# Kernel tuning notes

Hardware: AMD Instinct MI355X
Metric: run time of the kernel (lower is better)

Reference implementation:

```python
import jax, jax.numpy as jnp
import numpy as np

N_USER = 20000
N_ITEM = 20000
N = N_USER + N_ITEM          # total nodes
D = 128                      # n_hid (= in_feats = out_feats)
H = 4                        # GAT heads
L = 2                        # n_layers
M = 8                        # mem_size (hypernet bottleneck)
T = 5                        # num_rels in MemoryLayer
E_UI = 40000                 # user->item bipartite edges
E_T = 16000                  # homogeneous edges per relation type (grouped)
EPS = 1e-5


def _layer_norm(x, w, b):
    mu = x.mean(-1, keepdims=True)
    var = ((x - mu) ** 2).mean(-1, keepdims=True)
    return (x - mu) * jax.lax.rsqrt(var + EPS) * w + b


def _gat(h_src, h_dst, src_idx, dst_idx, n_dst, W, al, ar, bias):
    """DGL GATConv (shared fc, eval-mode dropout=identity, elu activation)."""
    fs = (h_src @ W.T).reshape(-1, H, D)          # [Ns, H, D]
    fd = (h_dst @ W.T).reshape(-1, H, D)          # [Nd, H, D]
    el = (fs * al).sum(-1)                        # [Ns, H]
    er = (fd * ar).sum(-1)                        # [Nd, H]
    e = jax.nn.leaky_relu(el[src_idx] + er[dst_idx], 0.2)   # [E, H]
    emax = jax.ops.segment_max(e, dst_idx, num_segments=n_dst)
    ex = jnp.exp(e - emax[dst_idx])
    denom = jax.ops.segment_sum(ex, dst_idx, num_segments=n_dst)
    a = ex / denom[dst_idx]                       # edge softmax per dst
    rst = jax.ops.segment_sum(a[:, :, None] * fs[src_idx], dst_idx, num_segments=n_dst)
    return jax.nn.elu(rst + bias.reshape(1, H, D))           # [Nd, H, D]


def _memory_layer(feat, edge_src, edge_dst, Wc, bc, Ww, nWc, nbc, nWw, h_bias, ln_w, ln_b):
    # edges grouped by relation type: edge_src/edge_dst are [T, E_T]
    hs = feat[edge_src]                           # [T, Et, D]
    hd = feat[edge_dst]                           # [T, Et, D]
    # per-edge hypernetwork: coef = LeakyReLU(Linear(dst)); w = Ww(coef); msg = w @ src
    coef = jax.nn.leaky_relu(jnp.einsum('ted,tmd->tem', hd, Wc) + bc[:, None, :], 0.2)
    tmp = jnp.einsum('tei,tmoi->temo', hs, Ww)    # [T, Et, M, D] -- M-bottleneck path
    msg = jnp.einsum('tem,temo->teo', coef, tmp)  # [T, Et, D]
    flat_dst = edge_dst.reshape(-1)
    s = jax.ops.segment_sum(msg.reshape(-1, D), flat_dst, num_segments=N)
    cnt = jax.ops.segment_sum(jnp.ones((flat_dst.shape[0],), feat.dtype), flat_dst, num_segments=N)
    agg = s / jnp.maximum(cnt, 1.0)[:, None]      # fn.mean (0 for isolated nodes)
    rep = _layer_norm(agg, ln_w, ln_b) + h_bias
    # self-loop node_ME(feat, feat)
    ncoef = jax.nn.leaky_relu(feat @ nWc.T + nbc, 0.2)       # [N, M]
    ntmp = jnp.einsum('ni,moi->nmo', feat, nWw)              # [N, M, D]
    rep = rep + jnp.einsum('nm,nmo->no', ncoef, ntmp)
    return jax.nn.leaky_relu(rep, 0.2)            # dropout = identity (eval)


def setup_inputs() -> dict:
    key = jax.random.key(0)
    ks = jax.random.split(key, 16)
    s = 0.05
    return {
        "embedding": jax.random.normal(ks[0], (N, D), jnp.float32),
        "gat_fc_W": jax.random.normal(ks[1], (L, 2, H * D, D), jnp.float32) * s,
        "gat_attn_l": jax.random.normal(ks[2], (L, 2, H, D), jnp.float32) * s,
        "gat_attn_r": jax.random.normal(ks[3], (L, 2, H, D), jnp.float32) * s,
        "gat_bias": jnp.zeros((L, 2, H * D), jnp.float32),
        "proj_W": jax.random.normal(ks[4], (L, 2, D, H * D), jnp.float32) * s,
        "proj_b": jnp.zeros((L, 2, D), jnp.float32),
        "mem_rel_Wc": jax.random.normal(ks[5], (L, T, M, D), jnp.float32) * s,
        "mem_rel_bc": jnp.zeros((L, T, M), jnp.float32),
        "mem_rel_Ww": jax.random.normal(ks[6], (L, T, M, D, D), jnp.float32) * s,
        "mem_node_Wc": jax.random.normal(ks[7], (L, M, D), jnp.float32) * s,
        "mem_node_bc": jnp.zeros((L, M), jnp.float32),
        "mem_node_Ww": jax.random.normal(ks[8], (L, M, D, D), jnp.float32) * s,
        "mem_h_bias": jnp.zeros((L, D), jnp.float32),
        "mem_ln_w": jnp.ones((L, D), jnp.float32),
        "mem_ln_b": jnp.zeros((L, D), jnp.float32),
        "final_ln_w": jnp.ones(((L + 1) * D,), jnp.float32),
        "final_ln_b": jnp.zeros(((L + 1) * D,), jnp.float32),
        "src_u": jax.random.randint(ks[9], (E_UI,), 0, N_USER, jnp.int32),
        "dst_i": jax.random.randint(ks[10], (E_UI,), 0, N_ITEM, jnp.int32),
        "edge_src": jax.random.randint(ks[11], (T, E_T), 0, N, jnp.int32),
        "edge_dst": jax.random.randint(ks[12], (T, E_T), 0, N, jnp.int32),
    }


def reference(embedding, gat_fc_W, gat_attn_l, gat_attn_r, gat_bias, proj_W, proj_b,
              mem_rel_Wc, mem_rel_bc, mem_rel_Ww, mem_node_Wc, mem_node_bc, mem_node_Ww,
              mem_h_bias, mem_ln_w, mem_ln_b, final_ln_w, final_ln_b,
              src_u, dst_i, edge_src, edge_dst):
    features = embedding
    all_emb = [features]
    for l in range(L):
        hu, hi = features[:N_USER], features[N_USER:]
        # relation 0: item -> user (dst = user)
        gu = _gat(hi, hu, dst_i, src_u, N_USER,
                  gat_fc_W[l, 0], gat_attn_l[l, 0], gat_attn_r[l, 0], gat_bias[l, 0])
        ru = jax.nn.elu(gu.reshape(N_USER, H * D) @ proj_W[l, 0].T + proj_b[l, 0])
        # relation 1: user -> item (dst = item)
        gi = _gat(hu, hi, src_u, dst_i, N_ITEM,
                  gat_fc_W[l, 1], gat_attn_l[l, 1], gat_attn_r[l, 1], gat_bias[l, 1])
        ri = jnp.asarray(jax.nn.elu(gi.reshape(N_ITEM, H * D) @ proj_W[l, 1].T + proj_b[l, 1]))
        trans = jnp.concatenate([ru, ri], axis=0)             # [N, D]
        mem = _memory_layer(all_emb[-1], edge_src, edge_dst,
                            mem_rel_Wc[l], mem_rel_bc[l], mem_rel_Ww[l],
                            mem_node_Wc[l], mem_node_bc[l], mem_node_Ww[l],
                            mem_h_bias[l], mem_ln_w[l], mem_ln_b[l])
        features = mem + trans
        all_emb.append(features)
    return _layer_norm(jnp.concatenate(all_emb, axis=1), final_ln_w, final_ln_b)
```

## Files before the change

kernel.cpp:

```cpp
#include <hip/hip_runtime.h>
#include <hip/hip_bf16.h>
#include <math.h>

typedef __hip_bfloat16 bf16;

#define NUSER 20000
#define NITEM 20000
#define NTOT  40000
#define DD    128
#define HH    4
#define TT    5
#define MMEM  8
#define EUI   40000
#define ET    16000

#define MP_N  40064
#define MP_H  20096

typedef __attribute__((ext_vector_type(8))) short short8;
typedef __attribute__((ext_vector_type(4))) float f32x4;

__device__ __forceinline__ void gload16(const bf16* g, bf16* l){
  __builtin_amdgcn_global_load_lds(
      (const __attribute__((address_space(1))) unsigned int*)g,
      (__attribute__((address_space(3))) unsigned int*)l, 16, 0, 0);
}
__device__ __forceinline__ float bu2f_lo(unsigned u){ return __uint_as_float(u << 16); }
__device__ __forceinline__ float bu2f_hi(unsigned u){ return __uint_as_float(u & 0xffff0000u); }

__device__ __forceinline__ int stage_cg(int lane){
  return (((lane&3) ^ ((lane>>2)&3) ^ (lane>>4)) << 3);
}
__device__ __forceinline__ int read_pc8(int lm, int lq){
  return ((lq ^ (lm&3) ^ ((lm>>2)&3)) << 3);
}

__global__ __launch_bounds__(256) void k_mfma_gemm(
    const bf16* __restrict__ A, const bf16* __restrict__ B,
    const float* __restrict__ bias, float* __restrict__ C,
    long Astr, long Bstr, long biasStr, long Cstr,
    int ldc, int M, int K, int act, int accum)
{
  A += (size_t)blockIdx.z*Astr; B += (size_t)blockIdx.z*Bstr;
  if (bias) bias += (size_t)blockIdx.z*biasStr;
  C += (size_t)blockIdx.z*Cstr;
  __shared__ bf16 As[128*32];
  __shared__ bf16 Bs[128*32];
  int tid = threadIdx.x;
  int wave = tid >> 6, lane = tid & 63;
  int r0 = blockIdx.x * 128, c0 = blockIdx.y * 128;
  int wm = (wave >> 1) * 64, wn = (wave & 1) * 64;
  f32x4 acc[4][4];
  #pragma unroll
  for (int i=0;i<4;i++)
    #pragma unroll
    for (int j=0;j<4;j++) acc[i][j] = (f32x4){0.f,0.f,0.f,0.f};

  int rq = lane >> 2;
  int cg = stage_cg(lane);
  const bf16* Ag = A + (size_t)(r0 + wave*32 + rq)*K + cg;
  const bf16* Bg = B + (size_t)(c0 + wave*32 + rq)*K + cg;
  bf16* AsW = As + wave*32*32;
  bf16* BsW = Bs + wave*32*32;
  int lm = lane & 15, lq = lane >> 4;
  int pc8 = read_pc8(lm, lq);
  const bf16* Ard = As + (wm + lm)*32 + pc8;
  const bf16* Brd = Bs + (wn + lm)*32 + pc8;

  for (int k0 = 0; k0 < K; k0 += 32){
    gload16(Ag + k0,            AsW);
    gload16(Ag + 16*K + k0,     AsW + 16*32);
    gload16(Bg + k0,            BsW);
    gload16(Bg + 16*K + k0,     BsW + 16*32);
    __syncthreads();
    short8 af[4], bfv[4];
    #pragma unroll
    for (int i=0;i<4;i++) af[i]  = *(const short8*)(Ard + i*16*32);
    #pragma unroll
    for (int j=0;j<4;j++) bfv[j] = *(const short8*)(Brd + j*16*32);
    #pragma unroll
    for (int i=0;i<4;i++)
      #pragma unroll
      for (int j=0;j<4;j++)
        acc[i][j] = __builtin_amdgcn_mfma_f32_16x16x32_bf16(af[i], bfv[j], acc[i][j], 0, 0, 0);
    __syncthreads();
  }
  #pragma unroll
  for (int i=0;i<4;i++){
    #pragma unroll
    for (int j=0;j<4;j++){
      int c = c0 + wn + j*16 + lm;
      #pragma unroll
      for (int rg=0; rg<4; rg++){
        int r = r0 + wm + i*16 + lq*4 + rg;
        if (r < M){
          float v = acc[i][j][rg];
          if (bias) v += bias[c];
          if (act==1) v = v>0.f ? v : expm1f(v);
          float* cp = &C[(size_t)r*ldc + c];
          if (accum) *cp += v; else *cp = v;
        }
      }
    }
  }
}

__global__ __launch_bounds__(256) void k_fc_gemm(
    const bf16* __restrict__ A, const bf16* __restrict__ B,
    bf16* __restrict__ Fb, const float* __restrict__ al, const float* __restrict__ ar,
    float* __restrict__ el, float* __restrict__ er, int M)
{
  __shared__ bf16 As[128*32];
  __shared__ bf16 Bs[128*32];
  __shared__ float redE[2][2][128];
  int tid = threadIdx.x;
  int wave = tid >> 6, lane = tid & 63;
  int h = blockIdx.y;
  int r0 = blockIdx.x * 128;
  int wm = (wave >> 1) * 64, wn = (wave & 1) * 64;
  f32x4 acc[4][4];
  #pragma unroll
  for (int i=0;i<4;i++)
    #pragma unroll
    for (int j=0;j<4;j++) acc[i][j] = (f32x4){0.f,0.f,0.f,0.f};

  int rq = lane >> 2;
  int cg = stage_cg(lane);
  const bf16* Ag = A + (size_t)(r0 + wave*32 + rq)*128 + cg;
  const bf16* Bg = B + (size_t)(h*128 + wave*32 + rq)*128 + cg;
  bf16* AsW = As + wave*32*32;
  bf16* BsW = Bs + wave*32*32;
  int lm = lane & 15, lq = lane >> 4;
  int pc8 = read_pc8(lm, lq);
  const bf16* Ard = As + (wm + lm)*32 + pc8;
  const bf16* Brd = Bs + (wn + lm)*32 + pc8;

  for (int k0 = 0; k0 < 128; k0 += 32){
    gload16(Ag + k0,             AsW);
    gload16(Ag + 16*128 + k0,    AsW + 16*32);
    gload16(Bg + k0,             BsW);
    gload16(Bg + 16*128 + k0,    BsW + 16*32);
    __syncthreads();
    short8 af[4], bfv[4];
    #pragma unroll
    for (int i=0;i<4;i++) af[i]  = *(const short8*)(Ard + i*16*32);
    #pragma unroll
    for (int j=0;j<4;j++) bfv[j] = *(const short8*)(Brd + j*16*32);
    #pragma unroll
    for (int i=0;i<4;i++)
      #pragma unroll
      for (int j=0;j<4;j++)
        acc[i][j] = __builtin_amdgcn_mfma_f32_16x16x32_bf16(af[i], bfv[j], acc[i][j], 0, 0, 0);
    __syncthreads();
  }
  float alv[4], arv[4];
  #pragma unroll
  for (int j=0;j<4;j++){
    int c = h*128 + wn + j*16 + lm;
    alv[j] = al[c]; arv[j] = ar[c];
  }
  int wnh = wave & 1;
  #pragma unroll
  for (int i=0;i<4;i++){
    #pragma unroll
    for (int rg=0; rg<4; rg++){
      float se = 0.f, sr = 0.f;
      #pragma unroll
      for (int j=0;j<4;j++){
        float v = acc[i][j][rg];
        se = fmaf(v, alv[j], se);
        sr = fmaf(v, arv[j], sr);
      }
      #pragma unroll
      for (int msk=1; msk<16; msk<<=1){
        se += __shfl_xor(se, msk);
        sr += __shfl_xor(sr, msk);
      }
      if (lm == 0){
        int rl = wm + i*16 + lq*4 + rg;
        redE[0][wnh][rl] = se;
        redE[1][wnh][rl] = sr;
      }
    }
  }
  #pragma unroll
  for (int i=0;i<4;i++){
    #pragma unroll
    for (int j=0;j<4;j++){
      int c = h*128 + wn + j*16 + lm;
      #pragma unroll
      for (int rg=0; rg<4; rg++){
        int r = r0 + wm + i*16 + lq*4 + rg;
        if (r < M) Fb[(size_t)r*512 + c] = __float2bfloat16(acc[i][j][rg]);
      }
    }
  }
  __syncthreads();
  if (tid < 128){
    int r = r0 + tid;
    if (r < M) el[(size_t)r*4 + h] = redE[0][0][tid] + redE[0][1][tid];
  } else {
    int t2 = tid - 128;
    int r = r0 + t2;
    if (r < M) er[(size_t)r*4 + h] = redE[1][0][t2] + redE[1][1][t2];
  }
}

__global__ __launch_bounds__(256) void k_memgemm(
    const float* __restrict__ feat, const int* __restrict__ src,
    const float* __restrict__ coef, const bf16* __restrict__ B,
    float* __restrict__ C, bf16* __restrict__ Cb,
    const float* __restrict__ trans, float* __restrict__ fout,
    long srcStr, long coefStr, long Bstr, long CbStr,
    int Mvalid, int mode)
{
  __shared__ bf16 Af[64*144];
  __shared__ float cfS[8*64];
  __shared__ bf16 Bs[2][128*32];
  int t = blockIdx.y;
  const int*   srcT  = src ? src + (size_t)t*srcStr : nullptr;
  const float* coefT = coef + (size_t)t*coefStr;
  const bf16*  Bt    = B + (size_t)t*Bstr;
  int tid = threadIdx.x, wave = tid >> 6, lane = tid & 63;
  int r0 = blockIdx.x * 64;

  {
    int rL = tid >> 2, seg = tid & 3;
    int r = r0 + rL;
    bool valid = r < Mvalid;
    int s = valid ? (srcT ? srcT[r] : r) : 0;
    const float4* fp = (const float4*)(feat + (size_t)s*128 + seg*32);
    bf16* ap = Af + rL*144 + seg*32;
    #pragma unroll
    for (int q=0;q<8;q+=2){
      float4 v0 = fp[q], v1 = fp[q+1];
      __hip_bfloat162 p0 = __float22bfloat162_rn(make_float2(v0.x, v0.y));
      __hip_bfloat162 p1 = __float22bfloat162_rn(make_float2(v0.z, v0.w));
      __hip_bfloat162 p2 = __float22bfloat162_rn(make_float2(v1.x, v1.y));
      __hip_bfloat162 p3 = __float22bfloat162_rn(make_float2(v1.z, v1.w));
      *(__hip_bfloat162*)(ap + q*4)     = p0;
      *(__hip_bfloat162*)(ap + q*4 + 2) = p1;
      *(__hip_bfloat162*)(ap + q*4 + 4) = p2;
      *(__hip_bfloat162*)(ap + q*4 + 6) = p3;
    }
  }
  if (tid < 64){
    int r = r0 + tid;
    bool valid = r < Mvalid;
    #pragma unroll
    for (int m=0;m<8;m++)
      cfS[m*64 + tid] = valid ? coefT[(size_t)r*8 + m] : 0.f;
  }

  int rq = lane >> 2;
  int cg = stage_cg(lane);
  const bf16* Bg0 = Bt + (size_t)(wave*32 + rq)*1024 + cg;
  const bf16* Bg1 = Bt + (size_t)(wave*32 + 16 + rq)*1024 + cg;

  int wm = (wave >> 1) * 32, wn = (wave & 1) * 64;
  int lm = lane & 15, lq = lane >> 4;
  int pc8 = read_pc8(lm, lq);

  f32x4 accC[2][4];
  #pragma unroll
  for (int i=0;i<2;i++)
    #pragma unroll
    for (int j=0;j<4;j++) accC[i][j] = (f32x4){0.f,0.f,0.f,0.f};

  {
    bf16* d = Bs[0] + wave*1024;
    gload16(Bg0, d);
    gload16(Bg1, d + 512);
  }
  __syncthreads();

  int buf = 0;
  #pragma unroll
  for (int m = 0; m < 8; m++){
    f32x4 accM[2][4];
    #pragma unroll
    for (int ic = 0; ic < 4; ic++){
      int kk = m*4 + ic;
      if (kk + 1 < 32){
        int k1 = (kk + 1) * 32;
        bf16* d = Bs[buf^1] + wave*1024;
        gload16(Bg0 + k1, d);
        gload16(Bg1 + k1, d + 512);
      }
      short8 af[2], bfv[4];
      #pragma unroll
      for (int i=0;i<2;i++)
        af[i] = *(const short8*)(Af + (size_t)(wm + i*16 + lm)*144 + ic*32 + lq*8);
      #pragma unroll
      for (int j=0;j<4;j++)
        bfv[j] = *(const short8*)(Bs[buf] + (wn + lm + j*16)*32 + pc8);
      if (ic == 0){
        #pragma unroll
        for (int i=0;i<2;i++)
          #pragma unroll
          for (int j=0;j<4;j++)
            accM[i][j] = __builtin_amdgcn_mfma_f32_16x16x32_bf16(af[i], bfv[j],
                             (f32x4){0.f,0.f,0.f,0.f}, 0, 0, 0);
      } else {
        #pragma unroll
        for (int i=0;i<2;i++)
          #pragma unroll
          for (int j=0;j<4;j++)
            accM[i][j] = __builtin_amdgcn_mfma_f32_16x16x32_bf16(af[i], bfv[j], accM[i][j], 0, 0, 0);
      }
      __syncthreads();
      buf ^= 1;
    }
    #pragma unroll
    for (int i=0;i<2;i++){
      f32x4 cf4 = *(const f32x4*)(cfS + m*64 + wm + i*16 + lq*4);
      #pragma unroll
      for (int j=0;j<4;j++)
        #pragma unroll
        for (int rg=0; rg<4; rg++)
          accC[i][j][rg] = fmaf(cf4[rg], accM[i][j][rg], accC[i][j][rg]);
    }
  }
  #pragma unroll
  for (int i=0;i<2;i++){
    #pragma unroll
    for (int j=0;j<4;j++){
      int c = wn + j*16 + lm;
      #pragma unroll
      for (int rg=0; rg<4; rg++){
        int r = r0 + wm + i*16 + lq*4 + rg;
        if (r < Mvalid){
          float v = accC[i][j][rg];
          if (mode == 0){
            Cb[(size_t)t*CbStr + (size_t)r*128 + c] = __float2bfloat16(v);
          } else {
            float x = C[(size_t)r*128 + c] + v;
            x = x>0.f ? x : 0.2f*x;
            fout[(size_t)r*128 + c] = x + trans[(size_t)r*128 + c];
          }
        }
      }
    }
  }
}

__global__ void k_f2b(const float* __restrict__ in, bf16* __restrict__ o, int nv, int nt){
  int i = blockIdx.x*256 + threadIdx.x;
  if (i < nt) o[i] = __float2bfloat16(i < nv ? in[i] : 0.f);
}

__global__ void k_repack(const float* __restrict__ in, bf16* __restrict__ o){
  int s = blockIdx.y;
  int g = blockIdx.x*256 + threadIdx.x;
  int m = g >> 14, od = (g >> 7) & 127, i = g & 127;
  o[(size_t)s*131072 + (size_t)od*1024 + m*128 + i] = __float2bfloat16(in[(size_t)s*131072 + g]);
}

__global__ void k_hist(const int* __restrict__ dIdx, int* __restrict__ cnt, int E){
  int e = blockIdx.x*256+threadIdx.x;
  if (e<E) atomicAdd(&cnt[dIdx[e]], 1);
}

__global__ __launch_bounds__(1024) void k_scan(const int* __restrict__ in,
                                               int* __restrict__ out, int n){
  __shared__ int wsum[16];
  __shared__ int carry;
  int tidx = threadIdx.x, lane = tidx & 63, w = tidx >> 6;
  if (tidx == 0) carry = 0;
  __syncthreads();
  for (int base = 0; base < n; base += 1024){
    int i = base + tidx;
    int v = (i < n) ? in[i] : 0;
    int x = v;
    #pragma unroll
    for (int off = 1; off < 64; off <<= 1){
      int t = __shfl_up(x, off);
      if (lane >= off) x += t;
    }
    if (lane == 63) wsum[w] = x;
    __syncthreads();
    if (w == 0 && lane < 16){
      int t = wsum[lane];
      #pragma unroll
      for (int off=1; off<16; off<<=1){
        int u = __shfl_up(t, off, 16);
        if (lane >= off) t += u;
      }
      wsum[lane] = t;
    }
    __syncthreads();
    int woff = (w == 0) ? 0 : wsum[w-1];
    int excl = carry + woff + x - v;
    if (i < n) out[i] = excl;
    __syncthreads();
    if (tidx == 1023) carry = carry + wsum[15];
    __syncthreads();
  }
  if (tidx == 0) out[n] = carry;
}

__global__ void k_csr_scatter(const int* __restrict__ sIdx, const int* __restrict__ dIdx,
                              int sOff, const int* __restrict__ rowptr,
                              int* __restrict__ cursor, int* __restrict__ col, int E){
  int e = blockIdx.x*256+threadIdx.x; if (e>=E) return;
  int d = dIdx[e];
  int pos = rowptr[d] + atomicAdd(&cursor[d], 1);
  col[pos] = sIdx[e] + sOff;
}

__global__ void k_csr_scatter_eid(const int* __restrict__ dIdx, const int* __restrict__ rowptr,
                                  int* __restrict__ cursor, int* __restrict__ col, int E){
  int e = blockIdx.x*256+threadIdx.x; if (e>=E) return;
  int d = dIdx[e];
  int pos = rowptr[d] + atomicAdd(&cursor[d], 1);
  col[pos] = e;
}

__global__ __launch_bounds__(64) void k_gat_gather(
    const int* __restrict__ rowptr, const int* __restrict__ col,
    const float* __restrict__ el, const float* __restrict__ er,
    const bf16* __restrict__ Fb, const float* __restrict__ gb,
    bf16* __restrict__ rstb, int dOff)
{
  int dl = blockIdx.x;
  int lane = threadIdx.x;
  int h = lane >> 4;
  int off = (lane & 15) << 3;
  float erh = er[(size_t)(dl + dOff)*4 + h];
  float m = -INFINITY, den = 0.f;
  float acc[8];
  #pragma unroll
  for (int i=0;i<8;i++) acc[i]=0.f;
  int jb = rowptr[dl], je = rowptr[dl+1];
  for (int j=jb; j<je; j++){
    int s = col[j];
    float e = el[(size_t)s*4+h] + erh;
    e = e > 0.f ? e : 0.2f*e;
    float mn = fmaxf(m, e);
    float sc = __expf(m - mn);
    float wj = __expf(e - mn);
    den = den*sc + wj;
    m = mn;
    uint4 u = *(const uint4*)(Fb + (size_t)s*512 + h*128 + off);
    acc[0]=acc[0]*sc + wj*bu2f_lo(u.x); acc[1]=acc[1]*sc + wj*bu2f_hi(u.x);
    acc[2]=acc[2]*sc + wj*bu2f_lo(u.y); acc[3]=acc[3]*sc + wj*bu2f_hi(u.y);
    acc[4]=acc[4]*sc + wj*bu2f_lo(u.z); acc[5]=acc[5]*sc + wj*bu2f_hi(u.z);
    acc[6]=acc[6]*sc + wj*bu2f_lo(u.w); acc[7]=acc[7]*sc + wj*bu2f_hi(u.w);
  }
  float inv = den > 0.f ? 1.f/den : 0.f;
  int cb = h*128 + off;
  float x[8];
  #pragma unroll
  for (int q=0;q<8;q++){
    float v = acc[q]*inv + gb[cb+q];
    x[q] = v>0.f ? v : expm1f(v);
  }
  union { uint4 u; __hip_bfloat162 p[4]; } O;
  #pragma unroll
  for (int q=0;q<4;q++) O.p[q] = __float22bfloat162_rn(make_float2(x[2*q], x[2*q+1]));
  *(uint4*)(rstb + (size_t)dl*512 + cb) = O.u;
}

__global__ void k_coef(const float* __restrict__ feat, const int* __restrict__ idx,
                       const float* __restrict__ Wc, const float* __restrict__ bc,
                       float* __restrict__ outc, int cnt){
  int t = blockIdx.y;
  __shared__ float wS[MMEM*DD];
  __shared__ float bS[MMEM];
  for (int i=threadIdx.x;i<MMEM*DD;i+=128) wS[i] = Wc[(size_t)t*MMEM*DD + i];
  if (threadIdx.x < MMEM) bS[threadIdx.x] = bc[t*MMEM + threadIdx.x];
  __syncthreads();
  int e = blockIdx.x*128 + threadIdx.x; if (e >= cnt) return;
  int node = idx ? idx[(size_t)t*cnt + e] : e;
  float acc[MMEM];
  #pragma unroll
  for (int m=0;m<MMEM;m++) acc[m]=bS[m];
  const float* fr = feat + (size_t)node*DD;
  for (int d2=0; d2<DD; d2++){
    float v = fr[d2];
    #pragma unroll
    for (int m=0;m<MMEM;m++) acc[m] = fmaf(v, wS[m*DD+d2], acc[m]);
  }
  float* op = outc + ((size_t)t*cnt + e)*MMEM;
  #pragma unroll
  for (int m=0;m<MMEM;m++){ float v=acc[m]; op[m] = v>0.f ? v : 0.2f*v; }
}

__global__ void k_mem_gather(const int* __restrict__ rpT, const int* __restrict__ colT,
                             const bf16* __restrict__ msg, float* __restrict__ sAgg){
  int n = blockIdx.x*4 + (threadIdx.x >> 6);
  if (n >= NTOT) return;
  int lane = threadIdx.x & 63;
  int jb = rpT[n], je = rpT[n+1];
  float a0=0.f, a1=0.f;
  for (int j=jb;j<je;j++){
    unsigned u = ((const unsigned*)(msg + (size_t)colT[j]*128))[lane];
    a0 += bu2f_lo(u); a1 += bu2f_hi(u);
  }
  *(float2*)(sAgg + (size_t)n*128 + lane*2) = make_float2(a0, a1);
}

__global__ void k_memln(const float* __restrict__ s, const int* __restrict__ rpT,
                        const float* __restrict__ lw, const float* __restrict__ lb,
                        const float* __restrict__ hb, float* __restrict__ outp){
  int n = blockIdx.x, lane = threadIdx.x;
  float c = fmaxf((float)(rpT[n+1]-rpT[n]), 1.f);
  float x1 = s[(size_t)n*128+lane]/c, x2 = s[(size_t)n*128+64+lane]/c;
  float t = x1+x2;
  #pragma unroll
  for (int off=32;off;off>>=1) t += __shfl_xor(t,off);
  float mu = t * (1.f/128.f);
  float d1=x1-mu, d2=x2-mu;
  float v = d1*d1+d2*d2;
  #pragma unroll
  for (int off=32;off;off>>=1) v += __shfl_xor(v,off);
  float r = rsqrtf(v*(1.f/128.f) + 1e-5f);
  outp[(size_t)n*128+lane]    = d1*r*lw[lane]    + lb[lane]    + hb[lane];
  outp[(size_t)n*128+64+lane] = d2*r*lw[64+lane] + lb[64+lane] + hb[64+lane];
}

__global__ void k_final_ln(const float* __restrict__ emb, const float* __restrict__ f1,
                           const float* __restrict__ f2, const float* __restrict__ w,
                           const float* __restrict__ b, float* __restrict__ out){
  int n = blockIdx.x, t = threadIdx.x;
  __shared__ float red[4];
  float x0 = emb[(size_t)n*128+t];
  float x1 = f1[(size_t)n*128+t];
  float x2 = f2[(size_t)n*128+t];
  float s = x0+x1+x2;
  #pragma unroll
  for (int off=32;off;off>>=1) s += __shfl_xor(s,off);
  if ((t&63)==0) red[t>>6] = s;
  __syncthreads();
  float mu = (red[0]+red[1]) * (1.f/384.f);
  float d0=x0-mu, d1=x1-mu, d2=x2-mu;
  float v = d0*d0+d1*d1+d2*d2;
  #pragma unroll
  for (int off=32;off;off>>=1) v += __shfl_xor(v,off);
  if ((t&63)==0) red[2+(t>>6)] = v;
  __syncthreads();
  float var = (red[2]+red[3]) * (1.f/384.f);
  float r = rsqrtf(var + 1e-5f);
  size_t o = (size_t)n*384;
  out[o+t]     = d0*r*w[t]     + b[t];
  out[o+128+t] = d1*r*w[128+t] + b[128+t];
  out[o+256+t] = d2*r*w[256+t] + b[256+t];
}

extern "C" void kernel_launch(void* const* d_in, const int* in_sizes, int n_in,
                              void* d_out, int out_size, void* d_ws, size_t ws_size,
                              hipStream_t stream)
{
  const float* emb   = (const float*)d_in[0];
  const float* fcW   = (const float*)d_in[1];
  const float* attl  = (const float*)d_in[2];
  const float* attr  = (const float*)d_in[3];
  const float* gbias = (const float*)d_in[4];
  const float* projW = (const float*)d_in[5];
  const float* projB = (const float*)d_in[6];
  const float* relWc = (const float*)d_in[7];
  const float* relbc = (const float*)d_in[8];
  const float* relWw = (const float*)d_in[9];
  const float* nodWc = (const float*)d_in[10];
  const float* nodbc = (const float*)d_in[11];
  const float* nodWw = (const float*)d_in[12];
  const float* hbias = (const float*)d_in[13];
  const float* mlnw  = (const float*)d_in[14];
  const float* mlnb  = (const float*)d_in[15];
  const float* flnw  = (const float*)d_in[16];
  const float* flnb  = (const float*)d_in[17];
  const int*  srcU  = (const int*)d_in[18];
  const int*  dstI  = (const int*)d_in[19];
  const int*  eSrc  = (const int*)d_in[20];
  const int*  eDst  = (const int*)d_in[21];
  float* out = (float*)d_out;

  char* wp = (char*)d_ws;
  auto alloc = [&](size_t bytes)->void* {
    void* p = (void*)wp; wp += (bytes + 511) & ~(size_t)511; return p;
  };
  float* feat1 = (float*)alloc((size_t)NTOT*DD*4);
  float* feat2 = (float*)alloc((size_t)NTOT*DD*4);
  float* Fbuf  = (float*)alloc((size_t)NTOT*512*4);
  float* rst   = (float*)alloc((size_t)NTOT*DD*2*4);
  bf16*  rstb0 = (bf16*)alloc((size_t)2*MP_H*512*2);
  float* trans = (float*)alloc((size_t)NTOT*DD*4);
  float* elF   = (float*)alloc((size_t)NTOT*4*4);
  float* erF   = (float*)alloc((size_t)NTOT*4*4);
  int* rpA  = (int*)alloc((size_t)(NUSER+1)*4);
  int* colA = (int*)alloc((size_t)EUI*4);
  int* rpB  = (int*)alloc((size_t)(NITEM+1)*4);
  int* colB = (int*)alloc((size_t)EUI*4);
  int* icnt = (int*)alloc((size_t)20000*4);
  int* icur = (int*)alloc((size_t)20000*4);
  int* rpT  = (int*)alloc((size_t)(NTOT+1)*4);
  int* colT = (int*)alloc((size_t)TT*ET*4);
  int* cntT = (int*)alloc((size_t)NTOT*4);
  int* icurT= (int*)alloc((size_t)NTOT*4);
  bf16* featb  = (bf16*)alloc((size_t)MP_N*DD*2);
  bf16* fcWb   = (bf16*)alloc((size_t)4*512*DD*2);
  bf16* projWb = (bf16*)alloc((size_t)4*DD*512*2);
  bf16* relWwb = (bf16*)alloc((size_t)10*DD*1024*2);
  bf16* nodWwb = (bf16*)alloc((size_t)2*DD*1024*2);
  bf16*  Fb     = (bf16*)Fbuf;
  bf16*  msgBb  = (bf16*)((char*)Fbuf + (size_t)NTOT*512*2);
  float* coefB  = (float*)((char*)msgBb + (size_t)TT*ET*128*2);
  float* ncoefB = coefB + (size_t)TT*ET*8;
  bf16*  rstb1  = rstb0 + (size_t)MP_H*512;
  float* sAgg   = rst;
  float* memO   = rst + (size_t)NTOT*DD;

  k_f2b<<<dim3((4*512*DD+255)/256),256,0,stream>>>(fcW, fcWb, 4*512*DD, 4*512*DD);
  k_f2b<<<dim3((4*DD*512+255)/256),256,0,stream>>>(projW, projWb, 4*DD*512, 4*DD*512);
  k_repack<<<dim3(512,10),256,0,stream>>>(relWw, relWwb);
  k_repack<<<dim3(512,2),256,0,stream>>>(nodWw, nodWwb);
  hipMemsetAsync(rstb0 + (size_t)20000*512, 0, (size_t)(MP_H-20000)*512*2, stream);
  hipMemsetAsync(rstb1 + (size_t)20000*512, 0, (size_t)(MP_H-20000)*512*2, stream);

  hipMemsetAsync(icnt, 0, 20000*4, stream);
  hipMemsetAsync(icur, 0, 20000*4, stream);
  k_hist<<<dim3((EUI+255)/256),256,0,stream>>>(srcU, icnt, EUI);
  k_scan<<<dim3(1),1024,0,stream>>>(icnt, rpA, NUSER);
  k_csr_scatter<<<dim3((EUI+255)/256),256,0,stream>>>(dstI, srcU, NUSER, rpA, icur, colA, EUI);
  hipMemsetAsync(icnt, 0, 20000*4, stream);
  hipMemsetAsync(icur, 0, 20000*4, stream);
  k_hist<<<dim3((EUI+255)/256),256,0,stream>>>(dstI, icnt, EUI);
  k_scan<<<dim3(1),1024,0,stream>>>(icnt, rpB, NITEM);
  k_csr_scatter<<<dim3((EUI+255)/256),256,0,stream>>>(srcU, dstI, 0, rpB, icur, colB, EUI);
  hipMemsetAsync(cntT, 0, NTOT*4, stream);
  hipMemsetAsync(icurT, 0, NTOT*4, stream);
  k_hist<<<dim3((TT*ET+255)/256),256,0,stream>>>(eDst, cntT, TT*ET);
  k_scan<<<dim3(1),1024,0,stream>>>(cntT, rpT, NTOT);
  k_csr_scatter_eid<<<dim3((TT*ET+255)/256),256,0,stream>>>(eDst, rpT, icurT, colT, TT*ET);

  const float* feats[3] = {emb, feat1, feat2};
  for (int l=0; l<2; l++){
    const float* fin  = feats[l];
    float* fout = (float*)feats[l+1];

    k_f2b<<<dim3((MP_N*DD+255)/256),256,0,stream>>>(fin, featb, NTOT*DD, MP_N*DD);

    for (int d=0; d<2; d++){
      k_fc_gemm<<<dim3(MP_N/128, 4),256,0,stream>>>(
          featb, fcWb + (size_t)(l*2+d)*512*DD, Fb,
          attl+(size_t)(l*2+d)*512, attr+(size_t)(l*2+d)*512, elF, erF, NTOT);
      int dOff = (d==0) ? 0 : NUSER;
      const int* rp  = (d==0) ? rpA : rpB;
      const int* col = (d==0) ? colA : colB;
      k_gat_gather<<<dim3(20000),64,0,stream>>>(rp, col, elF, erF, Fb,
          gbias+(size_t)(l*2+d)*512, (d==0) ? rstb0 : rstb1, dOff);
    }
    k_mfma_gemm<<<dim3(MP_H/128, 1, 2),256,0,stream>>>(
        rstb0, projWb + (size_t)(l*2)*DD*512, projB + (size_t)(l*2)*DD, trans,
        (long)MP_H*512, (long)DD*512, (long)DD, (long)20000*DD,
        DD, 20000, 512, 1, 0);

    k_coef<<<dim3((ET+127)/128, TT),128,0,stream>>>(fin, eDst,
        relWc+(size_t)l*TT*MMEM*DD, relbc+(size_t)l*TT*MMEM, coefB, ET);
    k_memgemm<<<dim3(ET/64, TT),256,0,stream>>>(
        fin, eSrc, coefB, relWwb + (size_t)l*TT*DD*1024,
        nullptr, msgBb, nullptr, nullptr,
        (long)ET, (long)ET*8, (long)DD*1024, (long)ET*128, ET, 0);
    k_mem_gather<<<dim3(NTOT/4),256,0,stream>>>(rpT, colT, msgBb, sAgg);
    k_memln<<<dim3(NTOT),64,0,stream>>>(sAgg, rpT, mlnw+(size_t)l*DD, mlnb+(size_t)l*DD,
                                        hbias+(size_t)l*DD, memO);
    k_coef<<<dim3((NTOT+127)/128, 1),128,0,stream>>>(fin, nullptr,
        nodWc+(size_t)l*MMEM*DD, nodbc+(size_t)l*MMEM, ncoefB, NTOT);
    k_memgemm<<<dim3(MP_N/64, 1),256,0,stream>>>(
        fin, nullptr, ncoefB, nodWwb + (size_t)l*DD*1024,
        memO, nullptr, trans, fout,
        0, 0, 0, 0, NTOT, 2);
  }

  k_final_ln<<<dim3(NTOT),128,0,stream>>>(emb, feat1, feat2, flnw, flnb, out);
}
```

Measured before the change: 957.9 us.

## Deepen memgemm B pipeline, keep A fragments in registers, vectorize coef kernel

```diff
diff --git a/kernel.cpp b/kernel.cpp
--- a/kernel.cpp
+++ b/kernel.cpp
@@ -206,7 +206,7 @@
   }
 }
 
-__global__ __launch_bounds__(256) void k_memgemm(
+__global__ __launch_bounds__(256,2) void k_memgemm(
     const float* __restrict__ feat, const int* __restrict__ src,
     const float* __restrict__ coef, const bf16* __restrict__ B,
     float* __restrict__ C, bf16* __restrict__ Cb,
@@ -214,34 +214,39 @@
     long srcStr, long coefStr, long Bstr, long CbStr,
     int Mvalid, int mode)
 {
-  __shared__ bf16 Af[64*144];
+  __shared__ bf16 Bs[4][2][128*32];
   __shared__ float cfS[8*64];
-  __shared__ bf16 Bs[2][128*32];
   int t = blockIdx.y;
   const int*   srcT  = src ? src + (size_t)t*srcStr : nullptr;
   const float* coefT = coef + (size_t)t*coefStr;
   const bf16*  Bt    = B + (size_t)t*Bstr;
   int tid = threadIdx.x, wave = tid >> 6, lane = tid & 63;
   int r0 = blockIdx.x * 64;
-
+  int wm = (wave >> 1) * 32, wn = (wave & 1) * 64;
+  int lm = lane & 15, lq = lane >> 4;
+
+  short8 afr[4][2];
   {
-    int rL = tid >> 2, seg = tid & 3;
-    int r = r0 + rL;
-    bool valid = r < Mvalid;
-    int s = valid ? (srcT ? srcT[r] : r) : 0;
-    const float4* fp = (const float4*)(feat + (size_t)s*128 + seg*32);
-    bf16* ap = Af + rL*144 + seg*32;
-    #pragma unroll
-    for (int q=0;q<8;q+=2){
-      float4 v0 = fp[q], v1 = fp[q+1];
-      __hip_bfloat162 p0 = __float22bfloat162_rn(make_float2(v0.x, v0.y));
-      __hip_bfloat162 p1 = __float22bfloat162_rn(make_float2(v0.z, v0.w));
-      __hip_bfloat162 p2 = __float22bfloat162_rn(make_float2(v1.x, v1.y));
-      __hip_bfloat162 p3 = __float22bfloat162_rn(make_float2(v1.z, v1.w));
-      *(__hip_bfloat162*)(ap + q*4)     = p0;
-      *(__hip_bfloat162*)(ap + q*4 + 2) = p1;
-      *(__hip_bfloat162*)(ap + q*4 + 4) = p2;
-      *(__hip_bfloat162*)(ap + q*4 + 6) = p3;
+    int r1 = r0 + wm + lm;
+    int r2 = r1 + 16;
+    int s1 = (r1 < Mvalid) ? (srcT ? srcT[r1] : r1) : 0;
+    int s2 = (r2 < Mvalid) ? (srcT ? srcT[r2] : r2) : 0;
+    const float4* f1 = (const float4*)(feat + (size_t)s1*128 + lq*8);
+    const float4* f2 = (const float4*)(feat + (size_t)s2*128 + lq*8);
+    #pragma unroll
+    for (int ic=0; ic<4; ic++){
+      float4 x0 = f1[ic*8], x1 = f1[ic*8+1];
+      float4 y0 = f2[ic*8], y1 = f2[ic*8+1];
+      union { short8 s8; __hip_bfloat162 p[4]; } u, v;
+      u.p[0]=__float22bfloat162_rn(make_float2(x0.x,x0.y));
+      u.p[1]=__float22bfloat162_rn(make_float2(x0.z,x0.w));
+      u.p[2]=__float22bfloat162_rn(make_float2(x1.x,x1.y));
+      u.p[3]=__float22bfloat162_rn(make_float2(x1.z,x1.w));
+      v.p[0]=__float22bfloat162_rn(make_float2(y0.x,y0.y));
+      v.p[1]=__float22bfloat162_rn(make_float2(y0.z,y0.w));
+      v.p[2]=__float22bfloat162_rn(make_float2(y1.x,y1.y));
+      v.p[3]=__float22bfloat162_rn(make_float2(y1.z,y1.w));
+      afr[ic][0]=u.s8; afr[ic][1]=v.s8;
     }
   }
   if (tid < 64){
@@ -256,71 +261,75 @@
   int cg = stage_cg(lane);
   const bf16* Bg0 = Bt + (size_t)(wave*32 + rq)*1024 + cg;
   const bf16* Bg1 = Bt + (size_t)(wave*32 + 16 + rq)*1024 + cg;
-
-  int wm = (wave >> 1) * 32, wn = (wave & 1) * 64;
-  int lm = lane & 15, lq = lane >> 4;
   int pc8 = read_pc8(lm, lq);
 
+#define ISSUE_B(p) do{                         \
+    int _b = (p)*64;                           \
+    bf16* _d = &Bs[(p)&3][0][wave*1024];       \
+    gload16(Bg0 + _b,       _d);               \
+    gload16(Bg1 + _b,       _d + 512);         \
+    gload16(Bg0 + _b + 32,  _d + 4096);        \
+    gload16(Bg1 + _b + 32,  _d + 4096 + 512);  \
+  }while(0)
+
+  ISSUE_B(0);
+  ISSUE_B(1);
+
   f32x4 accC[2][4];
   #pragma unroll
   for (int i=0;i<2;i++)
     #pragma unroll
     for (int j=0;j<4;j++) accC[i][j] = (f32x4){0.f,0.f,0.f,0.f};
-
-  {
-    bf16* d = Bs[0] + wave*1024;
-    gload16(Bg0, d);
-    gload16(Bg1, d + 512);
-  }
-  __syncthreads();
-
-  int buf = 0;
-  #pragma unroll
-  for (int m = 0; m < 8; m++){
-    f32x4 accM[2][4];
-    #pragma unroll
-    for (int ic = 0; ic < 4; ic++){
-      int kk = m*4 + ic;
-      if (kk + 1 < 32){
-        int k1 = (kk + 1) * 32;
-        bf16* d = Bs[buf^1] + wave*1024;
-        gload16(Bg0 + k1, d);
-        gload16(Bg1 + k1, d + 512);
-      }
-      short8 af[2], bfv[4];
-      #pragma unroll
-      for (int i=0;i<2;i++)
-        af[i] = *(const short8*)(Af + (size_t)(wm + i*16 + lm)*144 + ic*32 + lq*8);
+  f32x4 accM[2][4];
+
+  asm volatile("s_waitcnt lgkmcnt(0)" ::: "memory");
+
+  #pragma unroll
+  for (int p=0; p<16; p++){
+    if (p < 14) ISSUE_B(p+2);
+    if (p < 14)       asm volatile("s_waitcnt vmcnt(8)" ::: "memory");
+    else if (p == 14) asm volatile("s_waitcnt vmcnt(4)" ::: "memory");
+    else              asm volatile("s_waitcnt vmcnt(0)" ::: "memory");
+    __builtin_amdgcn_s_barrier();
+    asm volatile("" ::: "memory");
+    #pragma unroll
+    for (int s=0; s<2; s++){
+      int ic = ((p&1)<<1) + s;
+      const bf16* bsub = &Bs[p&3][s][0];
+      short8 bfv[4];
       #pragma unroll
       for (int j=0;j<4;j++)
-        bfv[j] = *(const short8*)(Bs[buf] + (wn + lm + j*16)*32 + pc8);
-      if (ic == 0){
+        bfv[j] = *(const short8*)(bsub + (wn + lm + j*16)*32 + pc8);
+      if ((p&1)==0 && s==0){
         #pragma unroll
         for (int i=0;i<2;i++)
           #pragma unroll
           for (int j=0;j<4;j++)
-            accM[i][j] = __builtin_amdgcn_mfma_f32_16x16x32_bf16(af[i], bfv[j],
+            accM[i][j] = __builtin_amdgcn_mfma_f32_16x16x32_bf16(afr[ic][i], bfv[j],
                              (f32x4){0.f,0.f,0.f,0.f}, 0, 0, 0);
       } else {
         #pragma unroll
         for (int i=0;i<2;i++)
           #pragma unroll
           for (int j=0;j<4;j++)
-            accM[i][j] = __builtin_amdgcn_mfma_f32_16x16x32_bf16(af[i], bfv[j], accM[i][j], 0, 0, 0);
-      }
-      __syncthreads();
-      buf ^= 1;
-    }
-    #pragma unroll
-    for (int i=0;i<2;i++){
-      f32x4 cf4 = *(const f32x4*)(cfS + m*64 + wm + i*16 + lq*4);
-      #pragma unroll
-      for (int j=0;j<4;j++)
+            accM[i][j] = __builtin_amdgcn_mfma_f32_16x16x32_bf16(afr[ic][i], bfv[j], accM[i][j], 0, 0, 0);
+      }
+    }
+    if (p & 1){
+      int m = p >> 1;
+      #pragma unroll
+      for (int i=0;i<2;i++){
+        f32x4 cf4 = *(const f32x4*)(cfS + m*64 + wm + i*16 + lq*4);
         #pragma unroll
-        for (int rg=0; rg<4; rg++)
-          accC[i][j][rg] = fmaf(cf4[rg], accM[i][j][rg], accC[i][j][rg]);
-    }
-  }
+        for (int j=0;j<4;j++)
+          #pragma unroll
+          for (int rg=0; rg<4; rg++)
+            accC[i][j][rg] = fmaf(cf4[rg], accM[i][j][rg], accC[i][j][rg]);
+      }
+    }
+  }
+#undef ISSUE_B
+
   #pragma unroll
   for (int i=0;i<2;i++){
     #pragma unroll
@@ -465,9 +474,12 @@
                        const float* __restrict__ Wc, const float* __restrict__ bc,
                        float* __restrict__ outc, int cnt){
   int t = blockIdx.y;
-  __shared__ float wS[MMEM*DD];
+  __shared__ float wT[DD*MMEM];
   __shared__ float bS[MMEM];
-  for (int i=threadIdx.x;i<MMEM*DD;i+=128) wS[i] = Wc[(size_t)t*MMEM*DD + i];
+  for (int i=threadIdx.x;i<MMEM*DD;i+=128){
+    int m = i >> 7, d = i & 127;
+    wT[d*MMEM + m] = Wc[(size_t)t*MMEM*DD + i];
+  }
   if (threadIdx.x < MMEM) bS[threadIdx.x] = bc[t*MMEM + threadIdx.x];
   __syncthreads();
   int e = blockIdx.x*128 + threadIdx.x; if (e >= cnt) return;
@@ -475,11 +487,18 @@
   float acc[MMEM];
   #pragma unroll
   for (int m=0;m<MMEM;m++) acc[m]=bS[m];
-  const float* fr = feat + (size_t)node*DD;
-  for (int d2=0; d2<DD; d2++){
-    float v = fr[d2];
-    #pragma unroll
-    for (int m=0;m<MMEM;m++) acc[m] = fmaf(v, wS[m*DD+d2], acc[m]);
+  const float4* fr = (const float4*)(feat + (size_t)node*DD);
+  for (int d4=0; d4<32; d4++){
+    float4 v = fr[d4];
+    const float* w0 = wT + d4*4*MMEM;
+    #pragma unroll
+    for (int m=0;m<MMEM;m++) acc[m] = fmaf(v.x, w0[m], acc[m]);
+    #pragma unroll
+    for (int m=0;m<MMEM;m++) acc[m] = fmaf(v.y, w0[MMEM+m], acc[m]);
+    #pragma unroll
+    for (int m=0;m<MMEM;m++) acc[m] = fmaf(v.z, w0[2*MMEM+m], acc[m]);
+    #pragma unroll
+    for (int m=0;m<MMEM;m++) acc[m] = fmaf(v.w, w0[3*MMEM+m], acc[m]);
   }
   float* op = outc + ((size_t)t*cnt + e)*MMEM;
   #pragma unroll
```

After: 1.153 ms. 1.2x slower.

## Load memgemm B fragments directly from global and vectorize coef kernel

Applied to the files above, without the earlier changes.

```diff
diff --git a/kernel.cpp b/kernel.cpp
--- a/kernel.cpp
+++ b/kernel.cpp
@@ -214,9 +214,8 @@
     long srcStr, long coefStr, long Bstr, long CbStr,
     int Mvalid, int mode)
 {
-  __shared__ bf16 Af[64*144];
+  __shared__ bf16 Af[64*136];
   __shared__ float cfS[8*64];
-  __shared__ bf16 Bs[2][128*32];
   int t = blockIdx.y;
   const int*   srcT  = src ? src + (size_t)t*srcStr : nullptr;
   const float* coefT = coef + (size_t)t*coefStr;
@@ -230,18 +229,14 @@
     bool valid = r < Mvalid;
     int s = valid ? (srcT ? srcT[r] : r) : 0;
     const float4* fp = (const float4*)(feat + (size_t)s*128 + seg*32);
-    bf16* ap = Af + rL*144 + seg*32;
+    bf16* ap = Af + rL*136 + seg*32;
     #pragma unroll
     for (int q=0;q<8;q+=2){
       float4 v0 = fp[q], v1 = fp[q+1];
-      __hip_bfloat162 p0 = __float22bfloat162_rn(make_float2(v0.x, v0.y));
-      __hip_bfloat162 p1 = __float22bfloat162_rn(make_float2(v0.z, v0.w));
-      __hip_bfloat162 p2 = __float22bfloat162_rn(make_float2(v1.x, v1.y));
-      __hip_bfloat162 p3 = __float22bfloat162_rn(make_float2(v1.z, v1.w));
-      *(__hip_bfloat162*)(ap + q*4)     = p0;
-      *(__hip_bfloat162*)(ap + q*4 + 2) = p1;
-      *(__hip_bfloat162*)(ap + q*4 + 4) = p2;
-      *(__hip_bfloat162*)(ap + q*4 + 6) = p3;
+      *(__hip_bfloat162*)(ap + q*4)     = __float22bfloat162_rn(make_float2(v0.x, v0.y));
+      *(__hip_bfloat162*)(ap + q*4 + 2) = __float22bfloat162_rn(make_float2(v0.z, v0.w));
+      *(__hip_bfloat162*)(ap + q*4 + 4) = __float22bfloat162_rn(make_float2(v1.x, v1.y));
+      *(__hip_bfloat162*)(ap + q*4 + 6) = __float22bfloat162_rn(make_float2(v1.z, v1.w));
     }
   }
   if (tid < 64){
@@ -251,15 +246,22 @@
     for (int m=0;m<8;m++)
       cfS[m*64 + tid] = valid ? coefT[(size_t)r*8 + m] : 0.f;
   }
-
-  int rq = lane >> 2;
-  int cg = stage_cg(lane);
-  const bf16* Bg0 = Bt + (size_t)(wave*32 + rq)*1024 + cg;
-  const bf16* Bg1 = Bt + (size_t)(wave*32 + 16 + rq)*1024 + cg;
+  __syncthreads();
 
   int wm = (wave >> 1) * 32, wn = (wave & 1) * 64;
   int lm = lane & 15, lq = lane >> 4;
-  int pc8 = read_pc8(lm, lq);
+
+  short8 afr[4][2];
+  #pragma unroll
+  for (int ic=0; ic<4; ic++)
+    #pragma unroll
+    for (int i=0; i<2; i++)
+      afr[ic][i] = *(const short8*)(Af + (size_t)(wm + i*16 + lm)*136 + ic*32 + lq*8);
+
+  const bf16* Bl0 = Bt + (size_t)(wn +  0 + lm)*1024 + lq*8;
+  const bf16* Bl1 = Bt + (size_t)(wn + 16 + lm)*1024 + lq*8;
+  const bf16* Bl2 = Bt + (size_t)(wn + 32 + lm)*1024 + lq*8;
+  const bf16* Bl3 = Bt + (size_t)(wn + 48 + lm)*1024 + lq*8;
 
   f32x4 accC[2][4];
   #pragma unroll
@@ -267,49 +269,31 @@
     #pragma unroll
     for (int j=0;j<4;j++) accC[i][j] = (f32x4){0.f,0.f,0.f,0.f};
 
-  {
-    bf16* d = Bs[0] + wave*1024;
-    gload16(Bg0, d);
-    gload16(Bg1, d + 512);
-  }
-  __syncthreads();
-
-  int buf = 0;
   #pragma unroll
   for (int m = 0; m < 8; m++){
     f32x4 accM[2][4];
     #pragma unroll
     for (int ic = 0; ic < 4; ic++){
-      int kk = m*4 + ic;
-      if (kk + 1 < 32){
-        int k1 = (kk + 1) * 32;
-        bf16* d = Bs[buf^1] + wave*1024;
-        gload16(Bg0 + k1, d);
-        gload16(Bg1 + k1, d + 512);
-      }
-      short8 af[2], bfv[4];
-      #pragma unroll
-      for (int i=0;i<2;i++)
-        af[i] = *(const short8*)(Af + (size_t)(wm + i*16 + lm)*144 + ic*32 + lq*8);
-      #pragma unroll
-      for (int j=0;j<4;j++)
-        bfv[j] = *(const short8*)(Bs[buf] + (wn + lm + j*16)*32 + pc8);
+      int ko = m*128 + ic*32;
+      short8 bfv[4];
+      bfv[0] = *(const short8*)(Bl0 + ko);
+      bfv[1] = *(const short8*)(Bl1 + ko);
+      bfv[2] = *(const short8*)(Bl2 + ko);
+      bfv[3] = *(const short8*)(Bl3 + ko);
       if (ic == 0){
         #pragma unroll
         for (int i=0;i<2;i++)
           #pragma unroll
           for (int j=0;j<4;j++)
-            accM[i][j] = __builtin_amdgcn_mfma_f32_16x16x32_bf16(af[i], bfv[j],
+            accM[i][j] = __builtin_amdgcn_mfma_f32_16x16x32_bf16(afr[ic][i], bfv[j],
                              (f32x4){0.f,0.f,0.f,0.f}, 0, 0, 0);
       } else {
         #pragma unroll
         for (int i=0;i<2;i++)
           #pragma unroll
           for (int j=0;j<4;j++)
-            accM[i][j] = __builtin_amdgcn_mfma_f32_16x16x32_bf16(af[i], bfv[j], accM[i][j], 0, 0, 0);
-      }
-      __syncthreads();
-      buf ^= 1;
+            accM[i][j] = __builtin_amdgcn_mfma_f32_16x16x32_bf16(afr[ic][i], bfv[j], accM[i][j], 0, 0, 0);
+      }
     }
     #pragma unroll
     for (int i=0;i<2;i++){
@@ -321,6 +305,7 @@
           accC[i][j][rg] = fmaf(cf4[rg], accM[i][j][rg], accC[i][j][rg]);
     }
   }
+
   #pragma unroll
   for (int i=0;i<2;i++){
     #pragma unroll
@@ -465,9 +450,12 @@
                        const float* __restrict__ Wc, const float* __restrict__ bc,
                        float* __restrict__ outc, int cnt){
   int t = blockIdx.y;
-  __shared__ float wS[MMEM*DD];
+  __shared__ float wT[DD*MMEM];
   __shared__ float bS[MMEM];
-  for (int i=threadIdx.x;i<MMEM*DD;i+=128) wS[i] = Wc[(size_t)t*MMEM*DD + i];
+  for (int i=threadIdx.x;i<MMEM*DD;i+=128){
+    int m = i >> 7, d = i & 127;
+    wT[d*MMEM + m] = Wc[(size_t)t*MMEM*DD + i];
+  }
   if (threadIdx.x < MMEM) bS[threadIdx.x] = bc[t*MMEM + threadIdx.x];
   __syncthreads();
   int e = blockIdx.x*128 + threadIdx.x; if (e >= cnt) return;
@@ -475,11 +463,18 @@
   float acc[MMEM];
   #pragma unroll
   for (int m=0;m<MMEM;m++) acc[m]=bS[m];
-  const float* fr = feat + (size_t)node*DD;
-  for (int d2=0; d2<DD; d2++){
-    float v = fr[d2];
-    #pragma unroll
-    for (int m=0;m<MMEM;m++) acc[m] = fmaf(v, wS[m*DD+d2], acc[m]);
+  const float4* fr = (const float4*)(feat + (size_t)node*DD);
+  for (int d4=0; d4<32; d4++){
+    float4 v = fr[d4];
+    const float* w0 = wT + d4*4*MMEM;
+    #pragma unroll
+    for (int m=0;m<MMEM;m++) acc[m] = fmaf(v.x, w0[m], acc[m]);
+    #pragma unroll
+    for (int m=0;m<MMEM;m++) acc[m] = fmaf(v.y, w0[MMEM+m], acc[m]);
+    #pragma unroll
+    for (int m=0;m<MMEM;m++) acc[m] = fmaf(v.z, w0[2*MMEM+m], acc[m]);
+    #pragma unroll
+    for (int m=0;m<MMEM;m++) acc[m] = fmaf(v.w, w0[3*MMEM+m], acc[m]);
   }
   float* op = outc + ((size_t)t*cnt + e)*MMEM;
   #pragma unroll
```

Result: slower. 1.021 ms (+6.6%).
